# Kernel tuning notes

Measured on AMD Instinct MI355X. Metric: run time of the kernel, lower is better.

The kernel has to match this reference:

```python
import jax, jax.numpy as jnp
import numpy as np

D_MODEL = 128
D_Q = 16
N_HEADS = 8
LEN_Q = 64
N_LAYERS = 2
F_DIM = 2048
GEST_F_DIM = 512
NUM_GEST = 16
T_FRAMES = 4096
LN_EPS = 1e-5


def _ln(x):
    # fresh nn.LayerNorm(d_model) each call in the torch code -> weight=1, bias=0
    m = jnp.mean(x, axis=-1, keepdims=True)
    v = jnp.var(x, axis=-1, keepdims=True)
    return (x - m) * jax.lax.rsqrt(v + LN_EPS)


def _mha(q_in, k_in, v_in, Wq, Wk, Wv, n_heads, d_q):
    # torch MultiHeadAttention_COG: note self.fc is defined but NOT applied;
    # output = context, then LayerNorm(context + residual)
    B, lq, _ = q_in.shape
    lk = k_in.shape[1]
    Q = (q_in @ Wq).reshape(B, lq, n_heads, d_q).transpose(0, 2, 1, 3)  # [B,h,lq,dq]
    K = (k_in @ Wk).reshape(B, lk, n_heads, d_q).transpose(0, 2, 1, 3)
    V = (v_in @ Wv).reshape(B, lk, n_heads, d_q).transpose(0, 2, 1, 3)
    scores = jnp.einsum('bhqd,bhkd->bhqk', Q, K) / jnp.sqrt(jnp.asarray(d_q, q_in.dtype))
    attn = jax.nn.softmax(scores, axis=-1)
    ctx = jnp.einsum('bhqk,bhkd->bhqd', attn, V)
    ctx = ctx.transpose(0, 2, 1, 3).reshape(B, lq, n_heads * d_q)
    return _ln(ctx + q_in)


def _ffn(x, W1, W2):
    # PoswiseFeedForwardNet: Linear->ReLU->Linear (bias=False), residual + fresh LN
    return _ln(jax.nn.relu(x @ W1) @ W2 + x)


def setup_inputs() -> dict:
    key = jax.random.key(0)
    ks = jax.random.split(key, 12)
    s = 0.02
    inp = {
        'g': jax.random.normal(ks[0], (1, NUM_GEST, GEST_F_DIM), jnp.float32),
        'long_feature': jax.random.normal(ks[1], (1, T_FRAMES, F_DIM), jnp.float32),
        'W_vis': jax.random.normal(ks[2], (F_DIM, D_MODEL), jnp.float32) * s,
        'W_txt': jax.random.normal(ks[3], (GEST_F_DIM, D_MODEL), jnp.float32) * s,
        'Wq_enc': jax.random.normal(ks[4], (N_LAYERS, D_MODEL, N_HEADS * D_Q), jnp.float32) * s,
        'Wk_enc': jax.random.normal(ks[5], (N_LAYERS, D_MODEL, N_HEADS * D_Q), jnp.float32) * s,
        'Wv_enc': jax.random.normal(ks[6], (N_LAYERS, D_MODEL, N_HEADS * D_Q), jnp.float32) * s,
        'W1_ffn': jax.random.normal(ks[7], (N_LAYERS, D_MODEL, F_DIM), jnp.float32) * s,
        'W2_ffn': jax.random.normal(ks[8], (N_LAYERS, F_DIM, D_MODEL), jnp.float32) * s,
        'Wq_f': jax.random.normal(ks[9], (D_MODEL, D_MODEL), jnp.float32) * s,
        'Wk_f': jax.random.normal(ks[10], (D_MODEL, D_MODEL), jnp.float32) * s,
        'Wv_f': jax.random.normal(ks[11], (D_MODEL, D_MODEL), jnp.float32) * s,
    }
    return inp


def reference(g, long_feature, W_vis, W_txt, Wq_enc, Wk_enc, Wv_enc,
              W1_ffn, W2_ffn, Wq_f, Wk_f, Wv_f):
    visual = long_feature[0] @ W_vis           # [T, d_model]
    text = g[0] @ W_txt                        # [num_gest, d_model]
    T = visual.shape[0]

    # per-frame causal window of length LEN_Q with zero left-padding (vectorized)
    padded = jnp.concatenate(
        [jnp.zeros((LEN_Q - 1, D_MODEL), visual.dtype), visual], axis=0)
    idx = jnp.arange(T)[:, None] + jnp.arange(LEN_Q)[None, :]  # [T, len_q]
    visual_feas = padded[idx]                                   # [T, len_q, d_model]
    text_feas = jnp.broadcast_to(text[None], (T, NUM_GEST, D_MODEL))

    # Encoder_COG: normalize visual once, then 2 cross-attn layers (Q=text, K=V=visual)
    vis = _ln(visual_feas)
    t = text_feas
    for l in range(N_LAYERS):
        tq = _ln(t)                                   # norm1
        t = _mha(tq, vis, vis, Wq_enc[l], Wk_enc[l], Wv_enc[l], N_HEADS, D_Q)
        t = _ffn(_ln(t), W1_ffn[l], W2_ffn[l])        # norm3 then FFN

    # final single-head attention: Q=enc_outputs, K=V=text, d_q=d_model
    dec = _mha(t, text_feas, text_feas, Wq_f, Wk_f, Wv_f, 1, D_MODEL)  # [T,num_gest,d_model]
    return dec.reshape(T, -1)[None]  # [1, T, num_gest*d_model]
```

## Files before the change

### kernel.cpp

```cpp
#include <hip/hip_runtime.h>
#include <math.h>

#define TFRAMES 4096
#define DM 128
#define LQ 64
#define NG 16
#define NH 8
#define DQH 16
#define FD 2048
#define GFD 512
#define PAD 63
#define KVROWS (TFRAMES + PAD)
#define ASTRIDE (KVROWS * DM)
#define FPB 4
#define MROWS (FPB * NG)
#define STS 136
#define VTS 72
#define PBS 72
#define UROWS (LQ + FPB - 1)

#define OFF_WVH  0
#define OFF_WVL  131072
#define OFF_WKVH 262144
#define OFF_WKVL 294912
#define OFF_KV   (TFRAMES * DM)
#define OFF_TEXT (OFF_KV + 2 * ASTRIDE)
#define OFF_KF   (OFF_TEXT + NG * DM)
#define OFF_VF   (OFF_KF + NG * DM)
#define OFF_W1T  (OFF_VF + NG * DM)
#define OFF_W2T  (OFF_W1T + 262144)
#define OFF_WQT  (OFF_W2T + 262144)
#define OFF_WQFT (OFF_WQT + 16384)

typedef __attribute__((ext_vector_type(8))) short bf16x8;
typedef __attribute__((ext_vector_type(4))) float f32x4;
#define MFMA16(a, b, c) __builtin_amdgcn_mfma_f32_16x16x32_bf16(a, b, c, 0, 0, 0)

__device__ __forceinline__ short bfc(float x) {
    union { float f; unsigned u; } v; v.f = x;
    unsigned r = v.u + 0x7fffu + ((v.u >> 16) & 1u);
    return (short)(r >> 16);
}
__device__ __forceinline__ float b2f(short s) {
    union { unsigned u; float f; } v;
    v.u = ((unsigned)(unsigned short)s) << 16;
    return v.f;
}
__device__ __forceinline__ bf16x8 shiftf(int4 a, int4 b, int f) {
    const int wo = f >> 1;
    const int sh = (f & 1) * 16;
    int w0 = wo ? a.y : a.x;
    int w1 = wo ? a.z : a.y;
    int w2 = wo ? a.w : a.z;
    int w3 = wo ? b.x : a.w;
    int w4 = wo ? b.y : b.x;
    int o0 = __builtin_amdgcn_alignbit(w1, w0, sh);
    int o1 = __builtin_amdgcn_alignbit(w2, w1, sh);
    int o2 = __builtin_amdgcn_alignbit(w3, w2, sh);
    int o3 = __builtin_amdgcn_alignbit(w4, w3, sh);
    int4 o = {o0, o1, o2, o3};
    return *(bf16x8*)&o;
}

__global__ __launch_bounds__(256) void k_wcvt(const float* __restrict__ Wq_enc,
                                              const float* __restrict__ W1f,
                                              const float* __restrict__ W2f,
                                              const float* __restrict__ Wqf,
                                              const float* __restrict__ Wk_enc,
                                              const float* __restrict__ Wv_enc,
                                              short* __restrict__ W1T,
                                              short* __restrict__ W2T,
                                              short* __restrict__ WQT,
                                              short* __restrict__ WQFT,
                                              short* __restrict__ WKVH,
                                              short* __restrict__ WKVL) {
    const int t = blockIdx.x * 256 + threadIdx.x;
    const int gsel = blockIdx.y;
    if (gsel < 2) {
        int n = t >> 7, k = t & 127;
        W1T[gsel * 262144 + t] = bfc(W1f[(size_t)gsel * 262144 + (size_t)k * FD + n]);
    } else if (gsel < 4) {
        int l = gsel - 2;
        int n = t >> 11, k = t & 2047;
        W2T[l * 262144 + t] = bfc(W2f[(size_t)l * 262144 + (size_t)k * DM + n]);
    } else if (gsel < 6) {
        int l = gsel - 4;
        if (t < 16384) {
            int n = t >> 7, k = t & 127;
            WQT[l * 16384 + t] = bfc(Wq_enc[(size_t)l * 16384 + k * DM + n]);
        }
    } else if (gsel == 6) {
        if (t < 16384) {
            int n = t >> 7, k = t & 127;
            WQFT[t] = bfc(Wqf[(size_t)k * DM + n]);
        }
    } else {
        if (t < 65536) {
            int a = t >> 14, rem = t & 16383;
            int n = rem >> 7, k = rem & 127;
            const float* src = ((a & 1) ? Wv_enc : Wk_enc) + (size_t)(a >> 1) * 16384;
            float v = src[k * 128 + n];
            short hi = bfc(v);
            WKVH[t] = hi;
            WKVL[t] = bfc(v - b2f(hi));
        }
    }
}

__global__ __launch_bounds__(256) void k_wvt(const float* __restrict__ Wvis,
                                             short* __restrict__ WVH,
                                             short* __restrict__ WVL) {
    __shared__ float tile[64][65];
    const int tid = threadIdx.x;
    const int k0 = blockIdx.x * 64;
    const int n0 = blockIdx.y * 64;
    for (int o = tid; o < 64 * 64; o += 256) {
        int r = o >> 6, c = o & 63;
        tile[r][c] = Wvis[(size_t)(k0 + r) * DM + n0 + c];
    }
    __syncthreads();
    for (int o = tid; o < 64 * 64; o += 256) {
        int rn = o >> 6, ck = o & 63;
        float v = tile[ck][rn];
        short hi = bfc(v);
        WVH[(size_t)(n0 + rn) * FD + k0 + ck] = hi;
        WVL[(size_t)(n0 + rn) * FD + k0 + ck] = bfc(v - b2f(hi));
    }
}

__global__ __launch_bounds__(256) void k_viskv(const float* __restrict__ lf,
                                               const short* __restrict__ WVH,
                                               const short* __restrict__ WVL,
                                               const short* __restrict__ WKVH,
                                               const short* __restrict__ WKVL,
                                               short* __restrict__ kvB) {
    __shared__ __align__(16) char smem[17408 + 4352];
    __shared__ float sPa[256], sPb[256], sMean[16], sRstd[16];
    short* Ah = (short*)smem;
    short* Al = (short*)(smem + 4352);
    float* vis = (float*)smem;
    short* Vh = (short*)(smem + 8704);
    short* Vl = (short*)(smem + 13056);

    const int tid = threadIdx.x;
    const int w = tid >> 6;
    const int lane = tid & 63;
    const int lq = lane & 15;
    const int quad = lane >> 4;
    const int r0 = blockIdx.x * 16;

    f32x4 acc[2];
    acc[0] = (f32x4){0.f, 0.f, 0.f, 0.f};
    acc[1] = (f32x4){0.f, 0.f, 0.f, 0.f};
    for (int c = 0; c < 16; ++c) {
        __syncthreads();
        for (int o = tid; o < 16 * 128; o += 256) {
            int r = o >> 7, j = o & 127;
            float v = lf[(size_t)(r0 + r) * FD + c * 128 + j];
            short hi = bfc(v);
            Ah[r * 136 + j] = hi;
            Al[r * 136 + j] = bfc(v - b2f(hi));
        }
        __syncthreads();
#pragma unroll
        for (int ks = 0; ks < 4; ++ks) {
            bf16x8 ah = *(const bf16x8*)&Ah[lq * 136 + ks * 32 + quad * 8];
            bf16x8 al = *(const bf16x8*)&Al[lq * 136 + ks * 32 + quad * 8];
#pragma unroll
            for (int nt = 0; nt < 2; ++nt) {
                const size_t bo = (size_t)(w * 32 + nt * 16 + lq) * FD + c * 128 + ks * 32 + quad * 8;
                bf16x8 bh = *(const bf16x8*)&WVH[bo];
                bf16x8 bl = *(const bf16x8*)&WVL[bo];
                acc[nt] = MFMA16(ah, bh, acc[nt]);
                acc[nt] = MFMA16(al, bh, acc[nt]);
                acc[nt] = MFMA16(ah, bl, acc[nt]);
            }
        }
    }
    __syncthreads();
#pragma unroll
    for (int nt = 0; nt < 2; ++nt)
#pragma unroll
        for (int r = 0; r < 4; ++r)
            vis[(quad * 4 + r) * 132 + w * 32 + nt * 16 + lq] = acc[nt][r];
    __syncthreads();

    {
        int row = tid >> 4, p = tid & 15;
        float s = 0.f, s2 = 0.f;
#pragma unroll
        for (int k = 0; k < 8; ++k) { float v = vis[row * 132 + p * 8 + k]; s += v; s2 += v * v; }
        sPa[tid] = s; sPb[tid] = s2;
    }
    __syncthreads();
    if (tid < 16) {
        float s = 0.f, s2 = 0.f;
#pragma unroll
        for (int p = 0; p < 16; ++p) { s += sPa[tid * 16 + p]; s2 += sPb[tid * 16 + p]; }
        float m = s * (1.f / 128.f);
        float v = s2 * (1.f / 128.f) - m * m;
        sMean[tid] = m; sRstd[tid] = rsqrtf(v + 1e-5f);
    }
    __syncthreads();
    for (int o = tid; o < 16 * 128; o += 256) {
        int r = o >> 7, j = o & 127;
        float v = (vis[r * 132 + j] - sMean[r]) * sRstd[r];
        short hi = bfc(v);
        Vh[r * 136 + j] = hi;
        Vl[r * 136 + j] = bfc(v - b2f(hi));
    }
    __syncthreads();

    for (int a = 0; a < 4; ++a) {
        f32x4 ka[2];
        ka[0] = (f32x4){0.f, 0.f, 0.f, 0.f};
        ka[1] = (f32x4){0.f, 0.f, 0.f, 0.f};
#pragma unroll
        for (int ks = 0; ks < 4; ++ks) {
            bf16x8 ah = *(const bf16x8*)&Vh[lq * 136 + ks * 32 + quad * 8];
            bf16x8 al = *(const bf16x8*)&Vl[lq * 136 + ks * 32 + quad * 8];
#pragma unroll
            for (int nt = 0; nt < 2; ++nt) {
                const size_t bo = (size_t)a * 16384 + (size_t)(w * 32 + nt * 16 + lq) * 128 + ks * 32 + quad * 8;
                bf16x8 bh = *(const bf16x8*)&WKVH[bo];
                bf16x8 bl = *(const bf16x8*)&WKVL[bo];
                ka[nt] = MFMA16(ah, bh, ka[nt]);
                ka[nt] = MFMA16(al, bh, ka[nt]);
                ka[nt] = MFMA16(ah, bl, ka[nt]);
            }
        }
#pragma unroll
        for (int nt = 0; nt < 2; ++nt)
#pragma unroll
            for (int r = 0; r < 4; ++r)
                kvB[(size_t)a * ASTRIDE + (size_t)(PAD + r0 + quad * 4 + r) * DM + w * 32 + nt * 16 + lq]
                    = bfc(ka[nt][r]);
    }
}

__global__ __launch_bounds__(128) void k_text(const float* __restrict__ g,
                                              const float* __restrict__ Wtxt,
                                              const float* __restrict__ Wkf,
                                              const float* __restrict__ Wvf,
                                              float* __restrict__ text,
                                              float* __restrict__ kf,
                                              float* __restrict__ vf) {
    __shared__ float gs[GFD];
    __shared__ float tr[DM];
    const int r = blockIdx.x;
    const int tid = threadIdx.x;
    for (int i = tid; i < GFD; i += 128) gs[i] = g[(size_t)r * GFD + i];
    __syncthreads();
    float acc = 0.f;
    for (int k = 0; k < GFD; ++k) acc += gs[k] * Wtxt[(size_t)k * DM + tid];
    tr[tid] = acc;
    text[(size_t)r * DM + tid] = acc;
    __syncthreads();
    float a1 = 0.f, a2 = 0.f;
    for (int k = 0; k < DM; ++k) {
        float x = tr[k];
        a1 += x * Wkf[(size_t)k * DM + tid];
        a2 += x * Wvf[(size_t)k * DM + tid];
    }
    kf[(size_t)r * DM + tid] = a1;
    vf[(size_t)r * DM + tid] = a2;
}

__device__ __forceinline__ void ln_stats64(const short* buf, int tid, int dbl,
                                           float* pa, float* pb, float* ms, float* rs) {
    {
        int row = tid >> 3, p = tid & 7;
        const bf16x8* bp = (const bf16x8*)(buf + row * STS + p * 16);
        float s = 0.f, s2 = 0.f;
#pragma unroll
        for (int q8 = 0; q8 < 2; ++q8) {
            bf16x8 x = bp[q8];
#pragma unroll
            for (int e = 0; e < 8; ++e) { float v = b2f(x[e]); s += v; s2 += v * v; }
        }
        pa[tid] = s; pb[tid] = s2;
    }
    __syncthreads();
    if (tid < 64) {
        float ss = 0.f, ss2 = 0.f;
#pragma unroll
        for (int p2 = 0; p2 < 8; ++p2) { ss += pa[tid * 8 + p2]; ss2 += pb[tid * 8 + p2]; }
        float m = ss * (1.f / 128.f);
        float v = ss2 * (1.f / 128.f) - m * m;
        float r = rsqrtf(v + 1e-5f);
        if (dbl) r *= rsqrtf(v / (v + 1e-5f) + 1e-5f);
        ms[tid] = m; rs[tid] = r;
    }
    __syncthreads();
}
__device__ __forceinline__ void ln_apply64(short* buf, int tid,
                                           const float* ms, const float* rs) {
    int row = tid >> 3, p = tid & 7;
    float m = ms[row], r = rs[row];
    bf16x8* bp = (bf16x8*)(buf + row * STS + p * 16);
#pragma unroll
    for (int q8 = 0; q8 < 2; ++q8) {
        bf16x8 x = bp[q8]; bf16x8 o;
#pragma unroll
        for (int e = 0; e < 8; ++e) o[e] = bfc((b2f(x[e]) - m) * r);
        bp[q8] = o;
    }
    __syncthreads();
}

__global__ __launch_bounds__(512, 4) void k_frames(
    const short* __restrict__ kvB,    const float* __restrict__ text,
    const float* __restrict__ kf,     const float* __restrict__ vf,
    const short* __restrict__ W1T,    const short* __restrict__ W2T,
    const short* __restrict__ WQT,    const short* __restrict__ WQFT,
    float* __restrict__ out) {
    __shared__ __align__(16) short sT[MROWS * STS];
    __shared__ __align__(16) short sX[MROWS * STS];
    __shared__ __align__(16) short sVT[128 * VTS];
    __shared__ __align__(16) short sPB[8 * 16 * PBS];
    __shared__ float sPa[512], sPb[512];
    __shared__ float sMean[64], sRstd[64];

    const int tid = threadIdx.x;
    const int w = tid >> 6;
    const int lane = tid & 63;
    const int lq = lane & 15;
    const int quad = lane >> 4;
    const int T0 = blockIdx.x * FPB;

    for (int o = tid; o < MROWS * 128; o += 512)
        sT[(o >> 7) * STS + (o & 127)] = bfc(text[((o >> 7) & 15) * 128 + (o & 127)]);
    __syncthreads();

    for (int l = 0; l < 2; ++l) {
        const short* kvK = kvB + (size_t)(2 * l) * ASTRIDE;
        const short* kvV = kvB + (size_t)(2 * l + 1) * ASTRIDE;

        for (int o = tid; o < UROWS * 128; o += 512) {
            int u = o >> 7, d = o & 127;
            sVT[d * VTS + u] = kvV[(size_t)(T0 + u) * 128 + d];
        }
        ln_stats64(sT, tid, 0, sPa, sPb, sMean, sRstd);

        {
            const short* wq = WQT + (size_t)l * 16384;
            bf16x8 B[4];
#pragma unroll
            for (int ks = 0; ks < 4; ++ks)
                B[ks] = *(const bf16x8*)&wq[(w * 16 + lq) * 128 + ks * 32 + quad * 8];
#pragma unroll
            for (int mt = 0; mt < 4; ++mt) {
                int row = mt * 16 + lq;
                float m = sMean[row], r = sRstd[row];
                f32x4 acc = {0.f, 0.f, 0.f, 0.f};
#pragma unroll
                for (int ks = 0; ks < 4; ++ks) {
                    bf16x8 t8 = *(const bf16x8*)&sT[row * STS + ks * 32 + quad * 8];
                    bf16x8 a8;
#pragma unroll
                    for (int e = 0; e < 8; ++e) a8[e] = bfc((b2f(t8[e]) - m) * r);
                    acc = MFMA16(a8, B[ks], acc);
                }
#pragma unroll
                for (int r4 = 0; r4 < 4; ++r4)
                    sX[(mt * 16 + quad * 4 + r4) * STS + w * 16 + lq] = bfc(acc[r4]);
            }
        }
        __syncthreads();

        {
            const int f = w >> 1;
            const int hg = (w & 1) * 4;
            short* Pb = sPB + w * 16 * PBS;
            bf16x8 zv = {};
            for (int hh = 0; hh < 4; ++hh) {
                const int h = hg + hh;
                bf16x8 aq;
                {
                    bf16x8 t8 = *(const bf16x8*)&sX[(f * 16 + lq) * STS + h * 16 + (quad & 1) * 8];
                    aq = (quad < 2) ? t8 : zv;
                }
                f32x4 sc4[4];
#pragma unroll
                for (int kt = 0; kt < 4; ++kt) {
                    bf16x8 bk = *(const bf16x8*)&kvK[(size_t)(T0 + f + kt * 16 + lq) * 128 + h * 16 + (quad & 1) * 8];
                    bk = (quad < 2) ? bk : zv;
                    f32x4 z4 = {0.f, 0.f, 0.f, 0.f};
                    sc4[kt] = MFMA16(aq, bk, z4);
                }
                float pr[4][4];
#pragma unroll
                for (int r = 0; r < 4; ++r) {
                    float a0 = sc4[0][r] * 0.25f, a1 = sc4[1][r] * 0.25f;
                    float a2 = sc4[2][r] * 0.25f, a3 = sc4[3][r] * 0.25f;
                    float mx = fmaxf(fmaxf(a0, a1), fmaxf(a2, a3));
                    mx = fmaxf(mx, __shfl_xor(mx, 1));
                    mx = fmaxf(mx, __shfl_xor(mx, 2));
                    mx = fmaxf(mx, __shfl_xor(mx, 4));
                    mx = fmaxf(mx, __shfl_xor(mx, 8));
                    float e0 = expf(a0 - mx), e1 = expf(a1 - mx);
                    float e2 = expf(a2 - mx), e3 = expf(a3 - mx);
                    float s = e0 + e1 + e2 + e3;
                    s += __shfl_xor(s, 1);
                    s += __shfl_xor(s, 2);
                    s += __shfl_xor(s, 4);
                    s += __shfl_xor(s, 8);
                    float inv = 1.f / s;
                    pr[r][0] = e0 * inv; pr[r][1] = e1 * inv;
                    pr[r][2] = e2 * inv; pr[r][3] = e3 * inv;
                }
                const short* vr = &sVT[(h * 16 + lq) * VTS];
                int4 v0 = *(const int4*)&vr[quad * 8];
                int4 v1 = *(const int4*)&vr[quad * 8 + 8];
                int4 u0 = *(const int4*)&vr[32 + quad * 8];
                int4 u1 = *(const int4*)&vr[32 + quad * 8 + 8];
                bf16x8 b0 = shiftf(v0, v1, f);
                bf16x8 b1 = shiftf(u0, u1, f);
                f32x4 ctx = {0.f, 0.f, 0.f, 0.f};
#pragma unroll
                for (int pass = 0; pass < 2; ++pass) {
#pragma unroll
                    for (int r = 0; r < 4; ++r)
#pragma unroll
                        for (int kt = 0; kt < 4; ++kt) {
                            float p = pr[r][kt];
                            short hi = bfc(p);
                            short v16 = pass == 0 ? hi : bfc(p - b2f(hi));
                            Pb[(quad * 4 + r) * PBS + kt * 16 + lq] = v16;
                        }
                    bf16x8 p0 = *(const bf16x8*)&Pb[lq * PBS + quad * 8];
                    bf16x8 p1 = *(const bf16x8*)&Pb[lq * PBS + 32 + quad * 8];
                    ctx = MFMA16(p0, b0, ctx);
                    ctx = MFMA16(p1, b1, ctx);
                }
#pragma unroll
                for (int r = 0; r < 4; ++r) {
                    int row = f * 16 + quad * 4 + r;
                    int col = h * 16 + lq;
                    float tq = (b2f(sT[row * STS + col]) - sMean[row]) * sRstd[row];
                    sT[row * STS + col] = bfc(ctx[r] + tq);
                }
            }
        }
        __syncthreads();

        ln_stats64(sT, tid, 1, sPa, sPb, sMean, sRstd);
        ln_apply64(sT, tid, sMean, sRstd);

        {
            const short* w1p = W1T + (size_t)l * 262144;
            const short* w2p = W2T + (size_t)l * 262144;
            bf16x8 XA[4][4];
#pragma unroll
            for (int mt = 0; mt < 4; ++mt)
#pragma unroll
                for (int ks = 0; ks < 4; ++ks)
                    XA[mt][ks] = *(const bf16x8*)&sT[(mt * 16 + lq) * STS + ks * 32 + quad * 8];
            f32x4 yacc[4];
#pragma unroll
            for (int mt = 0; mt < 4; ++mt) yacc[mt] = (f32x4){0.f, 0.f, 0.f, 0.f};
            for (int c = 0; c < 16; ++c) {
                {
                    f32x4 hacc[4];
#pragma unroll
                    for (int mt = 0; mt < 4; ++mt) hacc[mt] = (f32x4){0.f, 0.f, 0.f, 0.f};
#pragma unroll
                    for (int ks = 0; ks < 4; ++ks) {
                        bf16x8 B1 = *(const bf16x8*)&w1p[(size_t)(c * 128 + w * 16 + lq) * 128 + ks * 32 + quad * 8];
#pragma unroll
                        for (int mt = 0; mt < 4; ++mt) hacc[mt] = MFMA16(XA[mt][ks], B1, hacc[mt]);
                    }
#pragma unroll
                    for (int mt = 0; mt < 4; ++mt)
#pragma unroll
                        for (int r = 0; r < 4; ++r)
                            sX[(mt * 16 + quad * 4 + r) * STS + w * 16 + lq] = bfc(fmaxf(hacc[mt][r], 0.f));
                }
                __syncthreads();
#pragma unroll
                for (int ks = 0; ks < 4; ++ks) {
                    bf16x8 B2 = *(const bf16x8*)&w2p[(size_t)(w * 16 + lq) * 2048 + c * 128 + ks * 32 + quad * 8];
#pragma unroll
                    for (int mt = 0; mt < 4; ++mt) {
                        bf16x8 A = *(const bf16x8*)&sX[(mt * 16 + lq) * STS + ks * 32 + quad * 8];
                        yacc[mt] = MFMA16(A, B2, yacc[mt]);
                    }
                }
                __syncthreads();
            }
#pragma unroll
            for (int mt = 0; mt < 4; ++mt)
#pragma unroll
                for (int r = 0; r < 4; ++r) {
                    int row = mt * 16 + quad * 4 + r;
                    int col = w * 16 + lq;
                    sT[row * STS + col] = bfc(yacc[mt][r] + b2f(sT[row * STS + col]));
                }
        }
        __syncthreads();

        ln_stats64(sT, tid, 0, sPa, sPb, sMean, sRstd);
        ln_apply64(sT, tid, sMean, sRstd);
    }

    {
        bf16x8 B[4];
#pragma unroll
        for (int ks = 0; ks < 4; ++ks)
            B[ks] = *(const bf16x8*)&WQFT[(w * 16 + lq) * 128 + ks * 32 + quad * 8];
#pragma unroll
        for (int mt = 0; mt < 4; ++mt) {
            f32x4 acc = {0.f, 0.f, 0.f, 0.f};
#pragma unroll
            for (int ks = 0; ks < 4; ++ks) {
                bf16x8 A = *(const bf16x8*)&sT[(mt * 16 + lq) * STS + ks * 32 + quad * 8];
                acc = MFMA16(A, B[ks], acc);
            }
#pragma unroll
            for (int r = 0; r < 4; ++r)
                sX[(mt * 16 + quad * 4 + r) * STS + w * 16 + lq] = bfc(acc[r]);
        }
    }
    short* kfL = sPB;
    short* vfL = sPB + 16 * STS;
    float* scF = (float*)(sPB + 2 * 16 * STS);
    for (int o = tid; o < 2048; o += 512) {
        kfL[(o >> 7) * STS + (o & 127)] = bfc(kf[o]);
        vfL[(o >> 7) * STS + (o & 127)] = bfc(vf[o]);
    }
    __syncthreads();
    if (tid < 256) {
        int m = tid >> 2, kq = tid & 3;
        float a4[4] = {0.f, 0.f, 0.f, 0.f};
        for (int d8 = 0; d8 < 16; ++d8) {
            bf16x8 qc = *(const bf16x8*)&sX[m * STS + d8 * 8];
            float qf[8];
#pragma unroll
            for (int e = 0; e < 8; ++e) qf[e] = b2f(qc[e]);
#pragma unroll
            for (int k = 0; k < 4; ++k) {
                bf16x8 kc = *(const bf16x8*)&kfL[(kq * 4 + k) * STS + d8 * 8];
#pragma unroll
                for (int e = 0; e < 8; ++e) a4[k] += qf[e] * b2f(kc[e]);
            }
        }
#pragma unroll
        for (int k = 0; k < 4; ++k)
            scF[m * 17 + kq * 4 + k] = a4[k] * 0.08838834764831845f;
    }
    __syncthreads();
    if (tid < 64) {
        float* row = scF + tid * 17;
        float mx = row[0];
#pragma unroll
        for (int k = 1; k < 16; ++k) mx = fmaxf(mx, row[k]);
        float sum = 0.f;
#pragma unroll
        for (int k = 0; k < 16; ++k) { float e = expf(row[k] - mx); row[k] = e; sum += e; }
        float inv = 1.f / sum;
#pragma unroll
        for (int k = 0; k < 16; ++k) row[k] *= inv;
    }
    __syncthreads();
    {
        int jj = tid & 127, rr0 = tid >> 7;
        float vv[16];
#pragma unroll
        for (int k = 0; k < 16; ++k) vv[k] = b2f(vfL[k * STS + jj]);
#pragma unroll 4
        for (int rr = 0; rr < 16; ++rr) {
            int row = rr0 + 4 * rr;
            float acc = 0.f;
#pragma unroll
            for (int k = 0; k < 16; ++k) acc += scF[row * 17 + k] * vv[k];
            sX[row * STS + jj] = bfc(acc + b2f(sT[row * STS + jj]));
        }
    }
    __syncthreads();
    ln_stats64(sX, tid, 0, sPa, sPb, sMean, sRstd);
    for (int o = tid; o < MROWS * 128; o += 512) {
        int r = o >> 7;
        out[(size_t)T0 * 2048 + o] = (b2f(sX[r * STS + (o & 127)]) - sMean[r]) * sRstd[r];
    }
}

extern "C" void kernel_launch(void* const* d_in, const int* in_sizes, int n_in,
                              void* d_out, int out_size, void* d_ws, size_t ws_size,
                              hipStream_t stream) {
    const float* g      = (const float*)d_in[0];
    const float* lf     = (const float*)d_in[1];
    const float* Wvis   = (const float*)d_in[2];
    const float* Wtxt   = (const float*)d_in[3];
    const float* Wq_enc = (const float*)d_in[4];
    const float* Wk_enc = (const float*)d_in[5];
    const float* Wv_enc = (const float*)d_in[6];
    const float* W1f    = (const float*)d_in[7];
    const float* W2f    = (const float*)d_in[8];
    const float* Wqf    = (const float*)d_in[9];
    const float* Wkf    = (const float*)d_in[10];
    const float* Wvf    = (const float*)d_in[11];
    float* out = (float*)d_out;
    float* ws  = (float*)d_ws;

    short* WVH  = (short*)(ws + OFF_WVH);
    short* WVL  = (short*)(ws + OFF_WVL);
    short* WKVH = (short*)(ws + OFF_WKVH);
    short* WKVL = (short*)(ws + OFF_WKVL);
    short* kvB  = (short*)(ws + OFF_KV);
    float* text = ws + OFF_TEXT;
    float* kfp  = ws + OFF_KF;
    float* vfp  = ws + OFF_VF;
    short* W1T  = (short*)(ws + OFF_W1T);
    short* W2T  = (short*)(ws + OFF_W2T);
    short* WQT  = (short*)(ws + OFF_WQT);
    short* WQFT = (short*)(ws + OFF_WQFT);

    for (int a = 0; a < 4; ++a)
        hipMemsetAsync(kvB + (size_t)a * ASTRIDE, 0, (size_t)PAD * DM * sizeof(short), stream);

    k_wcvt <<<dim3(1024, 8), dim3(256), 0, stream>>>(Wq_enc, W1f, W2f, Wqf, Wk_enc, Wv_enc,
                                                     W1T, W2T, WQT, WQFT, WKVH, WKVL);
    k_wvt  <<<dim3(32, 2), dim3(256), 0, stream>>>(Wvis, WVH, WVL);
    k_viskv<<<dim3(TFRAMES / 16), dim3(256), 0, stream>>>(lf, WVH, WVL, WKVH, WKVL, kvB);
    k_text <<<dim3(NG), dim3(128), 0, stream>>>(g, Wtxt, Wkf, Wvf, text, kfp, vfp);
    k_frames<<<dim3(TFRAMES / FPB), dim3(512), 0, stream>>>(kvB, text, kfp, vfp, W1T, W2T, WQT, WQFT, out);
}
```

Before: 633.5 us.

## Restructure FFN into per-wave split-K tiles, prefetch loads, use packed bf16 converts

The FFN is reorganized so each wave owns a 16-row tile and half of the hidden dimension. Hidden activations stay in per-wave shared-memory scratch, which removes the two block-wide barriers per hidden chunk, and the two halves are summed through shared memory at the end. Separately, the visual projection kernel prefetches the next chunk of long_feature into registers, and bf16 conversions use the hardware packed convert instruction when the compiler provides it. Shared memory moves to one aliased pool. The trade-off is more per-wave register accumulators and more W1/W2 global loads per wave.

```diff
diff --git a/kernel.cpp b/kernel.cpp
--- a/kernel.cpp
+++ b/kernel.cpp
@@ -46,6 +46,20 @@
     v.u = ((unsigned)(unsigned short)s) << 16;
     return v.f;
 }
+#ifndef __has_builtin
+#define __has_builtin(x) 0
+#endif
+#if __has_builtin(__builtin_amdgcn_cvt_pk_bf16_f32)
+typedef __attribute__((ext_vector_type(2))) __bf16 bf2_t;
+__device__ __forceinline__ unsigned pkbf(float a, float b) {
+    bf2_t r = __builtin_amdgcn_cvt_pk_bf16_f32(a, b);
+    union { bf2_t v; unsigned u; } c; c.v = r; return c.u;
+}
+#else
+__device__ __forceinline__ unsigned pkbf(float a, float b) {
+    return (unsigned)(unsigned short)bfc(a) | ((unsigned)(unsigned short)bfc(b) << 16);
+}
+#endif
 __device__ __forceinline__ bf16x8 shiftf(int4 a, int4 b, int f) {
     const int wo = f >> 1;
     const int sh = (f & 1) * 16;
@@ -152,16 +166,31 @@
     f32x4 acc[2];
     acc[0] = (f32x4){0.f, 0.f, 0.f, 0.f};
     acc[1] = (f32x4){0.f, 0.f, 0.f, 0.f};
+    float pre[8];
+#pragma unroll
+    for (int i = 0; i < 8; ++i) {
+        int o = tid + 256 * i;
+        pre[i] = lf[(size_t)(r0 + (o >> 7)) * FD + (o & 127)];
+    }
     for (int c = 0; c < 16; ++c) {
         __syncthreads();
-        for (int o = tid; o < 16 * 128; o += 256) {
+#pragma unroll
+        for (int i = 0; i < 8; ++i) {
+            int o = tid + 256 * i;
             int r = o >> 7, j = o & 127;
-            float v = lf[(size_t)(r0 + r) * FD + c * 128 + j];
+            float v = pre[i];
             short hi = bfc(v);
             Ah[r * 136 + j] = hi;
             Al[r * 136 + j] = bfc(v - b2f(hi));
         }
         __syncthreads();
+        if (c < 15) {
+#pragma unroll
+            for (int i = 0; i < 8; ++i) {
+                int o = tid + 256 * i;
+                pre[i] = lf[(size_t)(r0 + (o >> 7)) * FD + (c + 1) * 128 + (o & 127)];
+            }
+        }
 #pragma unroll
         for (int ks = 0; ks < 4; ++ks) {
             bf16x8 ah = *(const bf16x8*)&Ah[lq * 136 + ks * 32 + quad * 8];
@@ -300,10 +329,13 @@
     bf16x8* bp = (bf16x8*)(buf + row * STS + p * 16);
 #pragma unroll
     for (int q8 = 0; q8 < 2; ++q8) {
-        bf16x8 x = bp[q8]; bf16x8 o;
-#pragma unroll
-        for (int e = 0; e < 8; ++e) o[e] = bfc((b2f(x[e]) - m) * r);
-        bp[q8] = o;
+        bf16x8 x = bp[q8];
+        unsigned u0 = pkbf((b2f(x[0]) - m) * r, (b2f(x[1]) - m) * r);
+        unsigned u1 = pkbf((b2f(x[2]) - m) * r, (b2f(x[3]) - m) * r);
+        unsigned u2 = pkbf((b2f(x[4]) - m) * r, (b2f(x[5]) - m) * r);
+        unsigned u3 = pkbf((b2f(x[6]) - m) * r, (b2f(x[7]) - m) * r);
+        int4 o = {(int)u0, (int)u1, (int)u2, (int)u3};
+        bp[q8] = *(bf16x8*)&o;
     }
     __syncthreads();
 }
@@ -314,12 +346,16 @@
     const short* __restrict__ W1T,    const short* __restrict__ W2T,
     const short* __restrict__ WQT,    const short* __restrict__ WQFT,
     float* __restrict__ out) {
-    __shared__ __align__(16) short sT[MROWS * STS];
-    __shared__ __align__(16) short sX[MROWS * STS];
-    __shared__ __align__(16) short sVT[128 * VTS];
-    __shared__ __align__(16) short sPB[8 * 16 * PBS];
-    __shared__ float sPa[512], sPb[512];
-    __shared__ float sMean[64], sRstd[64];
+    __shared__ __align__(16) char pool[76288];
+    short* sT  = (short*)pool;
+    short* sX  = (short*)(pool + 17408);
+    char*  R   = pool + 34816;
+    short* sVT = (short*)R;
+    short* sPB = (short*)(R + 18432);
+    float* sPa = (float*)(pool + 71680);
+    float* sPb = (float*)(pool + 73728);
+    float* sMean = (float*)(pool + 75776);
+    float* sRstd = (float*)(pool + 76032);
 
     const int tid = threadIdx.x;
     const int w = tid >> 6;
@@ -356,10 +392,12 @@
 #pragma unroll
                 for (int ks = 0; ks < 4; ++ks) {
                     bf16x8 t8 = *(const bf16x8*)&sT[row * STS + ks * 32 + quad * 8];
-                    bf16x8 a8;
-#pragma unroll
-                    for (int e = 0; e < 8; ++e) a8[e] = bfc((b2f(t8[e]) - m) * r);
-                    acc = MFMA16(a8, B[ks], acc);
+                    unsigned u0 = pkbf((b2f(t8[0]) - m) * r, (b2f(t8[1]) - m) * r);
+                    unsigned u1 = pkbf((b2f(t8[2]) - m) * r, (b2f(t8[3]) - m) * r);
+                    unsigned u2 = pkbf((b2f(t8[4]) - m) * r, (b2f(t8[5]) - m) * r);
+                    unsigned u3 = pkbf((b2f(t8[6]) - m) * r, (b2f(t8[7]) - m) * r);
+                    int4 ai = {(int)u0, (int)u1, (int)u2, (int)u3};
+                    acc = MFMA16(*(bf16x8*)&ai, B[ks], acc);
                 }
 #pragma unroll
                 for (int r4 = 0; r4 < 4; ++r4)
@@ -416,18 +454,20 @@
                 int4 u1 = *(const int4*)&vr[32 + quad * 8 + 8];
                 bf16x8 b0 = shiftf(v0, v1, f);
                 bf16x8 b1 = shiftf(u0, u1, f);
+                float hif[4][4];
+#pragma unroll
+                for (int r = 0; r < 4; ++r) {
+                    unsigned ha = pkbf(pr[r][0], pr[r][1]);
+                    unsigned hb = pkbf(pr[r][2], pr[r][3]);
+                    hif[r][0] = b2f((short)ha); hif[r][1] = b2f((short)(ha >> 16));
+                    hif[r][2] = b2f((short)hb); hif[r][3] = b2f((short)(hb >> 16));
+                    Pb[(quad * 4 + r) * PBS + 0  + lq] = (short)ha;
+                    Pb[(quad * 4 + r) * PBS + 16 + lq] = (short)(ha >> 16);
+                    Pb[(quad * 4 + r) * PBS + 32 + lq] = (short)hb;
+                    Pb[(quad * 4 + r) * PBS + 48 + lq] = (short)(hb >> 16);
+                }
                 f32x4 ctx = {0.f, 0.f, 0.f, 0.f};
-#pragma unroll
-                for (int pass = 0; pass < 2; ++pass) {
-#pragma unroll
-                    for (int r = 0; r < 4; ++r)
-#pragma unroll
-                        for (int kt = 0; kt < 4; ++kt) {
-                            float p = pr[r][kt];
-                            short hi = bfc(p);
-                            short v16 = pass == 0 ? hi : bfc(p - b2f(hi));
-                            Pb[(quad * 4 + r) * PBS + kt * 16 + lq] = v16;
-                        }
+                {
                     bf16x8 p0 = *(const bf16x8*)&Pb[lq * PBS + quad * 8];
                     bf16x8 p1 = *(const bf16x8*)&Pb[lq * PBS + 32 + quad * 8];
                     ctx = MFMA16(p0, b0, ctx);
@@ -435,10 +475,31 @@
                 }
 #pragma unroll
                 for (int r = 0; r < 4; ++r) {
-                    int row = f * 16 + quad * 4 + r;
+                    unsigned la = pkbf(pr[r][0] - hif[r][0], pr[r][1] - hif[r][1]);
+                    unsigned lb = pkbf(pr[r][2] - hif[r][2], pr[r][3] - hif[r][3]);
+                    Pb[(quad * 4 + r) * PBS + 0  + lq] = (short)la;
+                    Pb[(quad * 4 + r) * PBS + 16 + lq] = (short)(la >> 16);
+                    Pb[(quad * 4 + r) * PBS + 32 + lq] = (short)lb;
+                    Pb[(quad * 4 + r) * PBS + 48 + lq] = (short)(lb >> 16);
+                }
+                {
+                    bf16x8 p0 = *(const bf16x8*)&Pb[lq * PBS + quad * 8];
+                    bf16x8 p1 = *(const bf16x8*)&Pb[lq * PBS + 32 + quad * 8];
+                    ctx = MFMA16(p0, b0, ctx);
+                    ctx = MFMA16(p1, b1, ctx);
+                }
+                {
+                    int row0 = f * 16 + quad * 4;
                     int col = h * 16 + lq;
-                    float tq = (b2f(sT[row * STS + col]) - sMean[row]) * sRstd[row];
-                    sT[row * STS + col] = bfc(ctx[r] + tq);
+                    float z0 = ctx[0] + (b2f(sT[(row0 + 0) * STS + col]) - sMean[row0 + 0]) * sRstd[row0 + 0];
+                    float z1 = ctx[1] + (b2f(sT[(row0 + 1) * STS + col]) - sMean[row0 + 1]) * sRstd[row0 + 1];
+                    float z2 = ctx[2] + (b2f(sT[(row0 + 2) * STS + col]) - sMean[row0 + 2]) * sRstd[row0 + 2];
+                    float z3 = ctx[3] + (b2f(sT[(row0 + 3) * STS + col]) - sMean[row0 + 3]) * sRstd[row0 + 3];
+                    unsigned za = pkbf(z0, z1), zb = pkbf(z2, z3);
+                    sT[(row0 + 0) * STS + col] = (short)za;
+                    sT[(row0 + 1) * STS + col] = (short)(za >> 16);
+                    sT[(row0 + 2) * STS + col] = (short)zb;
+                    sT[(row0 + 3) * STS + col] = (short)(zb >> 16);
                 }
             }
         }
@@ -450,54 +511,71 @@
         {
             const short* w1p = W1T + (size_t)l * 262144;
             const short* w2p = W2T + (size_t)l * 262144;
-            bf16x8 XA[4][4];
-#pragma unroll
-            for (int mt = 0; mt < 4; ++mt)
-#pragma unroll
-                for (int ks = 0; ks < 4; ++ks)
-                    XA[mt][ks] = *(const bf16x8*)&sT[(mt * 16 + lq) * STS + ks * 32 + quad * 8];
-            f32x4 yacc[4];
-#pragma unroll
-            for (int mt = 0; mt < 4; ++mt) yacc[mt] = (f32x4){0.f, 0.f, 0.f, 0.f};
-            for (int c = 0; c < 16; ++c) {
-                {
-                    f32x4 hacc[4];
-#pragma unroll
-                    for (int mt = 0; mt < 4; ++mt) hacc[mt] = (f32x4){0.f, 0.f, 0.f, 0.f};
+            const int mw = w & 3, kw = w >> 2;
+            short* Hw = (short*)(R + w * 4352);
+            float* Yred = (float*)R;
+            bf16x8 XA[4];
+#pragma unroll
+            for (int ks = 0; ks < 4; ++ks)
+                XA[ks] = *(const bf16x8*)&sT[(mw * 16 + lq) * STS + ks * 32 + quad * 8];
+            f32x4 yacc[8];
+#pragma unroll
+            for (int nt = 0; nt < 8; ++nt) yacc[nt] = (f32x4){0.f, 0.f, 0.f, 0.f};
+            for (int cc = 0; cc < 8; ++cc) {
+                const int c = kw * 8 + cc;
+#pragma unroll
+                for (int nt = 0; nt < 8; ++nt) {
+                    f32x4 h = {0.f, 0.f, 0.f, 0.f};
 #pragma unroll
                     for (int ks = 0; ks < 4; ++ks) {
-                        bf16x8 B1 = *(const bf16x8*)&w1p[(size_t)(c * 128 + w * 16 + lq) * 128 + ks * 32 + quad * 8];
-#pragma unroll
-                        for (int mt = 0; mt < 4; ++mt) hacc[mt] = MFMA16(XA[mt][ks], B1, hacc[mt]);
+                        bf16x8 B1 = *(const bf16x8*)&w1p[(size_t)(c * 128 + nt * 16 + lq) * 128 + ks * 32 + quad * 8];
+                        h = MFMA16(XA[ks], B1, h);
                     }
-#pragma unroll
-                    for (int mt = 0; mt < 4; ++mt)
-#pragma unroll
-                        for (int r = 0; r < 4; ++r)
-                            sX[(mt * 16 + quad * 4 + r) * STS + w * 16 + lq] = bfc(fmaxf(hacc[mt][r], 0.f));
-                }
-                __syncthreads();
-#pragma unroll
-                for (int ks = 0; ks < 4; ++ks) {
-                    bf16x8 B2 = *(const bf16x8*)&w2p[(size_t)(w * 16 + lq) * 2048 + c * 128 + ks * 32 + quad * 8];
-#pragma unroll
-                    for (int mt = 0; mt < 4; ++mt) {
-                        bf16x8 A = *(const bf16x8*)&sX[(mt * 16 + lq) * STS + ks * 32 + quad * 8];
-                        yacc[mt] = MFMA16(A, B2, yacc[mt]);
+                    unsigned p01 = pkbf(fmaxf(h[0], 0.f), fmaxf(h[1], 0.f));
+                    unsigned p23 = pkbf(fmaxf(h[2], 0.f), fmaxf(h[3], 0.f));
+                    int cH = nt * 16 + lq;
+                    Hw[(quad * 4 + 0) * 136 + cH] = (short)p01;
+                    Hw[(quad * 4 + 1) * 136 + cH] = (short)(p01 >> 16);
+                    Hw[(quad * 4 + 2) * 136 + cH] = (short)p23;
+                    Hw[(quad * 4 + 3) * 136 + cH] = (short)(p23 >> 16);
+                }
+#pragma unroll
+                for (int ks2 = 0; ks2 < 4; ++ks2) {
+                    bf16x8 A = *(const bf16x8*)&Hw[lq * 136 + ks2 * 32 + quad * 8];
+#pragma unroll
+                    for (int nt = 0; nt < 8; ++nt) {
+                        bf16x8 B2 = *(const bf16x8*)&w2p[(size_t)(nt * 16 + lq) * 2048 + c * 128 + ks2 * 32 + quad * 8];
+                        yacc[nt] = MFMA16(A, B2, yacc[nt]);
                     }
                 }
-                __syncthreads();
-            }
-#pragma unroll
-            for (int mt = 0; mt < 4; ++mt)
-#pragma unroll
-                for (int r = 0; r < 4; ++r) {
-                    int row = mt * 16 + quad * 4 + r;
-                    int col = w * 16 + lq;
-                    sT[row * STS + col] = bfc(yacc[mt][r] + b2f(sT[row * STS + col]));
-                }
-        }
-        __syncthreads();
+            }
+            __syncthreads();
+            if (kw == 1) {
+#pragma unroll
+                for (int nt = 0; nt < 8; ++nt)
+#pragma unroll
+                    for (int r = 0; r < 4; ++r)
+                        Yred[(mw * 16 + quad * 4 + r) * 132 + nt * 16 + lq] = yacc[nt][r];
+            }
+            __syncthreads();
+            if (kw == 0) {
+#pragma unroll
+                for (int nt = 0; nt < 8; ++nt) {
+                    int col = nt * 16 + lq;
+                    int row0 = mw * 16 + quad * 4;
+                    float z0 = yacc[nt][0] + Yred[(row0 + 0) * 132 + col] + b2f(sT[(row0 + 0) * STS + col]);
+                    float z1 = yacc[nt][1] + Yred[(row0 + 1) * 132 + col] + b2f(sT[(row0 + 1) * STS + col]);
+                    float z2 = yacc[nt][2] + Yred[(row0 + 2) * 132 + col] + b2f(sT[(row0 + 2) * STS + col]);
+                    float z3 = yacc[nt][3] + Yred[(row0 + 3) * 132 + col] + b2f(sT[(row0 + 3) * STS + col]);
+                    unsigned za = pkbf(z0, z1), zb = pkbf(z2, z3);
+                    sT[(row0 + 0) * STS + col] = (short)za;
+                    sT[(row0 + 1) * STS + col] = (short)(za >> 16);
+                    sT[(row0 + 2) * STS + col] = (short)zb;
+                    sT[(row0 + 3) * STS + col] = (short)(zb >> 16);
+                }
+            }
+            __syncthreads();
+        }
 
         ln_stats64(sT, tid, 0, sPa, sPb, sMean, sRstd);
         ln_apply64(sT, tid, sMean, sRstd);
```

Result: slower. 1.259 ms (+98.7%).
